# Optimization experiments

Measured on AMD Instinct MI355X. Metric: run time of the kernel, lower is better.

The kernel has to match this reference:

```python
import jax, jax.numpy as jnp
import numpy as np

N = 102400      # total agents across all groups
GROUP = 50      # agents per group
G = N // GROUP  # 2048 groups
E = 128         # embedding_dim
H = 512         # h_dim


def setup_inputs() -> dict:
    key = jax.random.key(0)
    k1, k2, k3, k4, k5, k6 = jax.random.split(key, 6)
    hist_enc = jax.random.normal(k1, (N, H), dtype=jnp.float32)
    hist_pos_batch = jax.random.normal(k2, (N, 2), dtype=jnp.float32)
    # group boundaries: 0, 50, 100, ..., N  (len = G+1)
    seq_start_end = (jnp.arange(G + 1, dtype=jnp.int32) * GROUP)
    # spatial_embedding: Linear(2, E)
    Ws = jax.random.normal(k3, (2, E), dtype=jnp.float32) * (1.0 / np.sqrt(2.0))
    bs = jax.random.normal(k4, (E,), dtype=jnp.float32) * 0.01
    # mlp_pre_pool: Linear(E + H, H)
    Wm = jax.random.normal(k5, (E + H, H), dtype=jnp.float32) * (1.0 / np.sqrt(E + H))
    bm = jax.random.normal(k6, (H,), dtype=jnp.float32) * 0.01
    return {
        "hist_enc": hist_enc,
        "hist_pos_batch": hist_pos_batch,
        "seq_start_end": seq_start_end,
        "Ws": Ws, "bs": bs, "Wm": Wm, "bm": bm,
    }


def reference(hist_enc, hist_pos_batch, seq_start_end, Ws, bs, Wm, bm):
    # The original torch loop builds all n^2 pairs per group but keeps only
    # curr_pool_h[0:1], i.e. row i=0 -> pooled vector for the group's FIRST agent.
    # rel[i=0, j] = pos[j] - pos[start]; hidden index is j; max over j.
    n = hist_enc.shape[0]
    num_groups = seq_start_end.shape[0] - 1
    # segment id of each agent: group g covers [sse[g], sse[g+1])
    seg_ids = jnp.searchsorted(seq_start_end, jnp.arange(n, dtype=seq_start_end.dtype), side="right") - 1
    starts = seq_start_end[:-1]                      # [G]
    anchor = hist_pos_batch[starts][seg_ids]         # [N,2] pos of group's first agent
    rel = hist_pos_batch - anchor                    # [N,2]
    emb = jax.nn.relu(rel @ Ws + bs)                 # [N,E]
    h_in = jnp.concatenate([hist_enc, emb], axis=1)  # [N,E+H]
    pooled = jax.nn.relu(h_in @ Wm + bm)             # [N,H]
    out = jax.ops.segment_max(pooled, seg_ids, num_segments=num_groups)  # [G,H]
    return out
```

## Files before the change

### kernel.cpp

```cpp
#include <hip/hip_runtime.h>


typedef __bf16 bf16x8 __attribute__((ext_vector_type(8)));
typedef float floatx4 __attribute__((ext_vector_type(4)));

constexpr int NR = 102400;
constexpr int NG = 2048;
constexpr int E  = 128;
constexpr int H  = 512;
constexpr int KD = 640;
constexpr int BM = 128, BN = 128, BK = 32;

__device__ inline unsigned short f2bf(float f) {
    unsigned u = __float_as_uint(f);
    u += 0x7FFF + ((u >> 16) & 1u);
    return (unsigned short)(u >> 16);
}

__device__ inline unsigned pk2(float lo, float hi) {
    return __builtin_amdgcn_perm(__float_as_uint(hi) + 0x8000u,
                                 __float_as_uint(lo) + 0x8000u, 0x07060302u);
}

__device__ inline void async16(const void* g, void* l) {
    __builtin_amdgcn_global_load_lds(
        (const __attribute__((address_space(1))) unsigned int*)g,
        (__attribute__((address_space(3))) unsigned int*)l, 16, 0, 0);
}

__global__ __launch_bounds__(256) void prep2(
    const float* __restrict__ hist_enc, const float* __restrict__ pos,
    const int* __restrict__ sse, const float* __restrict__ Ws,
    const float* __restrict__ bs, const float* __restrict__ Wm,
    unsigned short* __restrict__ WmT, unsigned short* __restrict__ Abf,
    int* __restrict__ segArr, int doAbf)
{
    const int b = blockIdx.x;
    const int t = threadIdx.x;
    if (doAbf && b < 3200) {
        __shared__ float relRow[32][2];
        const int rowBase = b * 32;
        if (t < 32) {
            const int i = rowBase + t;
            int l = 0, r = NG + 1;
            while (l < r) { int m = (l + r) >> 1; if (sse[m] <= i) l = m + 1; else r = m; }
            const int g = l - 1;
            if (segArr) segArr[i] = g;
            const int a = sse[g];
            relRow[t][0] = pos[2 * i + 0] - pos[2 * a + 0];
            relRow[t][1] = pos[2 * i + 1] - pos[2 * a + 1];
        }
        __syncthreads();
#pragma unroll
        for (int j = 0; j < 8; ++j) {
            const int c = j * 256 + t;
            const int row = c >> 6, col = (c & 63) * 8;
            const float4 f0 = *(const float4*)&hist_enc[(size_t)(rowBase + row) * H + col];
            const float4 f1 = *(const float4*)&hist_enc[(size_t)(rowBase + row) * H + col + 4];
            uint4 u;
            u.x = pk2(f0.x, f0.y); u.y = pk2(f0.z, f0.w);
            u.z = pk2(f1.x, f1.y); u.w = pk2(f1.z, f1.w);
            *(uint4*)&Abf[(size_t)(rowBase + row) * KD + col] = u;
        }
#pragma unroll
        for (int j = 0; j < 2; ++j) {
            const int c = j * 256 + t;
            const int row = c >> 4, e = (c & 15) * 8;
            const float r0 = relRow[row][0], r1 = relRow[row][1];
            const float4 w0a = *(const float4*)&Ws[e],     w0b = *(const float4*)&Ws[e + 4];
            const float4 w1a = *(const float4*)&Ws[E + e], w1b = *(const float4*)&Ws[E + e + 4];
            const float4 ba  = *(const float4*)&bs[e],     bb  = *(const float4*)&bs[e + 4];
            const float v0 = fmaxf(r0 * w0a.x + r1 * w1a.x + ba.x, 0.f);
            const float v1 = fmaxf(r0 * w0a.y + r1 * w1a.y + ba.y, 0.f);
            const float v2 = fmaxf(r0 * w0a.z + r1 * w1a.z + ba.z, 0.f);
            const float v3 = fmaxf(r0 * w0a.w + r1 * w1a.w + ba.w, 0.f);
            const float v4 = fmaxf(r0 * w0b.x + r1 * w1b.x + bb.x, 0.f);
            const float v5 = fmaxf(r0 * w0b.y + r1 * w1b.y + bb.y, 0.f);
            const float v6 = fmaxf(r0 * w0b.z + r1 * w1b.z + bb.z, 0.f);
            const float v7 = fmaxf(r0 * w0b.w + r1 * w1b.w + bb.w, 0.f);
            uint4 u;
            u.x = pk2(v0, v1); u.y = pk2(v2, v3);
            u.z = pk2(v4, v5); u.w = pk2(v6, v7);
            *(uint4*)&Abf[(size_t)(rowBase + row) * KD + H + e] = u;
        }
    } else {
        const int bb = doAbf ? (b - 3200) : b;
        if (bb < 0 || bb >= 80) return;
        __shared__ float tile[64][65];
        const int kb = (bb % 10) * 64, nb = (bb / 10) * 64;
        const int tx = t & 63, tq = t >> 6;
#pragma unroll
        for (int i = 0; i < 16; ++i) {
            const int k = tq * 16 + i;
            tile[k][tx] = Wm[(size_t)(kb + k) * H + nb + tx];
        }
        __syncthreads();
#pragma unroll
        for (int i = 0; i < 16; ++i) {
            const int n = tq * 16 + i;
            WmT[(size_t)(nb + n) * KD + kb + tx] = f2bf(tile[tx][n]);
        }
    }
}

__global__ __launch_bounds__(256) void pool_mfma6(
    const unsigned short* __restrict__ Abf,
    const int*   __restrict__ sse,
    const int*   __restrict__ segArr,
    const unsigned short* __restrict__ WmT,
    const float* __restrict__ bm,
    float*       __restrict__ out)
{
    __shared__ __attribute__((aligned(16))) unsigned short As2[2][BM * BK];
    __shared__ __attribute__((aligned(16))) unsigned short Bs2[2][BN * BK];
    __shared__ int segRow[BM];
    __shared__ int bnd[3];
    __shared__ int Pmax[4][BN + 4];

    const int t = threadIdx.x;
    const int bid     = blockIdx.x;
    const int rowTile = (bid >> 5) * 8 + (bid & 7);
    const int colTile = (bid >> 3) & 3;
    const int rowBase = rowTile * BM;
    const int cTile   = colTile * BN;

    const int lane  = t & 63;
    const int wv    = t >> 6;
    const int wr    = (wv >> 1) * 64;
    const int wc    = (wv & 1) * 64;
    const int lcol  = lane & 15;
    const int lquad = lane >> 4;

    const int sRow0 = wv * 32 + (lane >> 2);
    const int sRow1 = sRow0 + 16;
    const int phys  = lane & 3;
    const int cl0   = phys ^ ((sRow0 >> 1) & 3);
    const int cl1   = phys ^ ((sRow1 >> 1) & 3);
    const unsigned short* gA0 = Abf + (size_t)(rowBase + sRow0) * KD + cl0 * 8;
    const unsigned short* gA1 = Abf + (size_t)(rowBase + sRow1) * KD + cl1 * 8;
    const unsigned short* gB0 = WmT + (size_t)(cTile + sRow0) * KD + cl0 * 8;
    const unsigned short* gB1 = WmT + (size_t)(cTile + sRow1) * KD + cl1 * 8;

    auto issue = [&](int kt, int buf) {
        const int ko = kt * BK;
        async16(gA0 + ko, &As2[buf][wv * 1024]);
        async16(gA1 + ko, &As2[buf][wv * 1024 + 512]);
        async16(gB0 + ko, &Bs2[buf][wv * 1024]);
        async16(gB1 + ko, &Bs2[buf][wv * 1024 + 512]);
    };

    issue(0, 0);

    if (segArr) {
        if (t < BM) segRow[t] = segArr[rowBase + t];
    } else if (t < BM) {
        const int i = rowBase + t;
        int l = 0, r = NG + 1;
        while (l < r) { int m = (l + r) >> 1; if (sse[m] <= i) l = m + 1; else r = m; }
        segRow[t] = l - 1;
    }
    if (t >= BM && t < BM + 3) bnd[t - BM] = BM;
    for (int idx = t; idx < 4 * (BN + 4); idx += 256) ((int*)Pmax)[idx] = 0;
    __syncthreads();
    if (t < BM - 1) {
        const int s0 = segRow[t], s1 = segRow[t + 1];
        if (s1 != s0) bnd[s1 - segRow[0] - 1] = t + 1;
    }

    floatx4 acc[4][4];
#pragma unroll
    for (int m = 0; m < 4; ++m)
#pragma unroll
        for (int n = 0; n < 4; ++n) acc[m][n] = (floatx4){0.f, 0.f, 0.f, 0.f};

    for (int kt = 0; kt < KD / BK; ++kt) {
        __syncthreads();
        if (kt < KD / BK - 1) issue(kt + 1, (kt + 1) & 1);

        const unsigned short* A = As2[kt & 1];
        const unsigned short* B = Bs2[kt & 1];
        bf16x8 af[4], bfr[4];
#pragma unroll
        for (int mt = 0; mt < 4; ++mt) {
            const int R = wr + mt * 16 + lcol;
            const int pc = lquad ^ ((R >> 1) & 3);
            af[mt] = *(const bf16x8*)&A[R * 32 + pc * 8];
        }
#pragma unroll
        for (int nt = 0; nt < 4; ++nt) {
            const int R = wc + nt * 16 + lcol;
            const int pc = lquad ^ ((R >> 1) & 3);
            bfr[nt] = *(const bf16x8*)&B[R * 32 + pc * 8];
        }
#pragma unroll
        for (int mt = 0; mt < 4; ++mt)
#pragma unroll
            for (int nt = 0; nt < 4; ++nt)
                acc[mt][nt] = __builtin_amdgcn_mfma_f32_16x16x32_bf16(af[mt], bfr[nt], acc[mt][nt], 0, 0, 0);
    }

    const int b0 = bnd[0], b1 = bnd[1], b2 = bnd[2];
    const int segBase = segRow[0];

#pragma unroll
    for (int nt = 0; nt < 4; ++nt) {
        const int col  = wc + nt * 16 + lcol;
        const float bias = bm[cTile + col];
        float pm[4] = {0.f, 0.f, 0.f, 0.f};
#pragma unroll
        for (int mt = 0; mt < 4; ++mt) {
#pragma unroll
            for (int r = 0; r < 4; ++r) {
                const int lr = wr + mt * 16 + lquad * 4 + r;
                const int ls = (lr >= b0) + (lr >= b1) + (lr >= b2);
                const float v = fmaxf(acc[mt][nt][r] + bias, 0.f);
                pm[ls] = fmaxf(pm[ls], v);
            }
        }
#pragma unroll
        for (int ls = 0; ls < 4; ++ls)
            if (pm[ls] > 0.f)
                atomicMax(&Pmax[ls][col], __float_as_int(pm[ls]));
    }
    __syncthreads();

    for (int idx = t; idx < 4 * BN; idx += 256) {
        const int ls = idx >> 7, col = idx & 127;
        if (ls > 0 && bnd[ls - 1] >= BM) continue;
        const int seg = segBase + ls;
        const int v   = Pmax[ls][col];
        const int gs  = sse[seg], ge = sse[seg + 1];
        float* dst = &out[(size_t)seg * H + cTile + col];
        if (gs >= rowBase && ge <= rowBase + BM) {
            *dst = __int_as_float(v);
        } else {
            atomicMax((int*)dst, v);
        }
    }
}

constexpr int LDAF = 40;
__global__ __launch_bounds__(256) void pool_mfma_fb(
    const float* __restrict__ hist_enc, const float* __restrict__ pos,
    const int* __restrict__ sse, const float* __restrict__ Ws,
    const float* __restrict__ bs, const unsigned short* __restrict__ WmT,
    const float* __restrict__ bm, float* __restrict__ out)
{
    __shared__ __attribute__((aligned(16))) unsigned short As[BM][LDAF];
    __shared__ __attribute__((aligned(16))) unsigned short Bs[BN][LDAF];
    __shared__ float relRow[BM][2];
    __shared__ int   segRow[BM];
    __shared__ int   bnd[3];
    __shared__ int   Pmax[4][BN + 4];

    const int t = threadIdx.x;
    const int cTile = blockIdx.x * BN;
    const int rowBase = blockIdx.y * BM;

    if (t < BM) {
        const int i = rowBase + t;
        int l = 0, r = NG + 1;
        while (l < r) { int m = (l + r) >> 1; if (sse[m] <= i) l = m + 1; else r = m; }
        const int g = l - 1;
        segRow[t] = g;
        const int a = sse[g];
        relRow[t][0] = pos[2 * i + 0] - pos[2 * a + 0];
        relRow[t][1] = pos[2 * i + 1] - pos[2 * a + 1];
    }
    if (t >= BM && t < BM + 3) bnd[t - BM] = BM;
    for (int idx = t; idx < 4 * (BN + 4); idx += 256) ((int*)Pmax)[idx] = 0;
    __syncthreads();
    if (t < BM - 1) {
        const int s0 = segRow[t], s1 = segRow[t + 1];
        if (s1 != s0) bnd[s1 - segRow[0] - 1] = t + 1;
    }

    const int lane = t & 63, wv = t >> 6;
    const int wr = (wv >> 1) * 64, wc = (wv & 1) * 64;
    const int lcol = lane & 15, lquad = lane >> 4;

    floatx4 acc[4][4];
#pragma unroll
    for (int m = 0; m < 4; ++m)
#pragma unroll
        for (int n = 0; n < 4; ++n) acc[m][n] = (floatx4){0.f, 0.f, 0.f, 0.f};

    for (int kt = 0; kt < KD / BK; ++kt) {
        const int k0 = kt * BK;
        float4 av[4]; uint4 bv[2];
        if (k0 < H) {
#pragma unroll
            for (int i = 0; i < 4; ++i) {
                const int idx = i * 256 + t;
                const int row = idx >> 3, kq = (idx & 7) * 4;
                av[i] = *(const float4*)&hist_enc[(size_t)(rowBase + row) * H + k0 + kq];
            }
        } else {
#pragma unroll
            for (int i = 0; i < 4; ++i) {
                const int idx = i * 256 + t;
                const int row = idx >> 3, kq = (idx & 7) * 4;
                const int e = k0 - H + kq;
                const float4 w0 = *(const float4*)&Ws[e];
                const float4 w1 = *(const float4*)&Ws[E + e];
                const float4 b4 = *(const float4*)&bs[e];
                const float r0 = relRow[row][0], r1 = relRow[row][1];
                av[i].x = fmaxf(r0 * w0.x + r1 * w1.x + b4.x, 0.f);
                av[i].y = fmaxf(r0 * w0.y + r1 * w1.y + b4.y, 0.f);
                av[i].z = fmaxf(r0 * w0.z + r1 * w1.z + b4.z, 0.f);
                av[i].w = fmaxf(r0 * w0.w + r1 * w1.w + b4.w, 0.f);
            }
        }
#pragma unroll
        for (int i = 0; i < 2; ++i) {
            const int idx = i * 256 + t;
            const int n = idx >> 2, q = idx & 3;
            bv[i] = *(const uint4*)&WmT[(size_t)(cTile + n) * KD + k0 + q * 8];
        }
        __syncthreads();
#pragma unroll
        for (int i = 0; i < 4; ++i) {
            const int idx = i * 256 + t;
            const int row = idx >> 3, kq = (idx & 7) * 4;
            ushort4 p;
            p.x = f2bf(av[i].x); p.y = f2bf(av[i].y);
            p.z = f2bf(av[i].z); p.w = f2bf(av[i].w);
            *(ushort4*)&As[row][kq] = p;
        }
#pragma unroll
        for (int i = 0; i < 2; ++i) {
            const int idx = i * 256 + t;
            const int n = idx >> 2, q = idx & 3;
            *(uint4*)&Bs[n][q * 8] = bv[i];
        }
        __syncthreads();

        bf16x8 af[4], bfr[4];
#pragma unroll
        for (int mt = 0; mt < 4; ++mt)
            af[mt] = *(const bf16x8*)&As[wr + mt * 16 + lcol][lquad * 8];
#pragma unroll
        for (int nt = 0; nt < 4; ++nt)
            bfr[nt] = *(const bf16x8*)&Bs[wc + nt * 16 + lcol][lquad * 8];
#pragma unroll
        for (int mt = 0; mt < 4; ++mt)
#pragma unroll
            for (int nt = 0; nt < 4; ++nt)
                acc[mt][nt] = __builtin_amdgcn_mfma_f32_16x16x32_bf16(af[mt], bfr[nt], acc[mt][nt], 0, 0, 0);
    }

    const int b0 = bnd[0], b1 = bnd[1], b2 = bnd[2];
    const int segBase = segRow[0];
#pragma unroll
    for (int nt = 0; nt < 4; ++nt) {
        const int col = wc + nt * 16 + lcol;
        const float bias = bm[cTile + col];
        float pm[4] = {0.f, 0.f, 0.f, 0.f};
#pragma unroll
        for (int mt = 0; mt < 4; ++mt) {
#pragma unroll
            for (int r = 0; r < 4; ++r) {
                const int lr = wr + mt * 16 + lquad * 4 + r;
                const int ls = (lr >= b0) + (lr >= b1) + (lr >= b2);
                const float v = fmaxf(acc[mt][nt][r] + bias, 0.f);
                pm[ls] = fmaxf(pm[ls], v);
            }
        }
#pragma unroll
        for (int ls = 0; ls < 4; ++ls)
            if (pm[ls] > 0.f) atomicMax(&Pmax[ls][col], __float_as_int(pm[ls]));
    }
    __syncthreads();
    for (int idx = t; idx < 4 * BN; idx += 256) {
        const int ls = idx >> 7, col = idx & 127;
        if (ls > 0 && bnd[ls - 1] >= BM) continue;
        const int seg = segBase + ls;
        const int v = Pmax[ls][col];
        const int gs = sse[seg], ge = sse[seg + 1];
        float* dst = &out[(size_t)seg * H + cTile + col];
        if (gs >= rowBase && ge <= rowBase + BM) *dst = __int_as_float(v);
        else atomicMax((int*)dst, v);
    }
}

extern "C" void kernel_launch(void* const* d_in, const int* in_sizes, int n_in,
                              void* d_out, int out_size, void* d_ws, size_t ws_size,
                              hipStream_t stream) {
    const float* hist_enc = (const float*)d_in[0];
    const float* pos      = (const float*)d_in[1];
    const int*   sse      = (const int*)  d_in[2];
    const float* Ws       = (const float*)d_in[3];
    const float* bs       = (const float*)d_in[4];
    const float* Wm       = (const float*)d_in[5];
    const float* bm       = (const float*)d_in[6];
    float*       out      = (float*)d_out;

    const size_t needWmT = (size_t)H * KD * 2;
    const size_t needA   = (size_t)NR * KD * 2;
    const size_t needSeg = (size_t)NR * 4;
    unsigned short* WmT  = (unsigned short*)d_ws;
    unsigned short* Abf  = (unsigned short*)((char*)d_ws + needWmT);
    int*            segA = (int*)((char*)d_ws + needWmT + needA);

    hipMemsetAsync(out, 0, (size_t)out_size * sizeof(float), stream);

    if (ws_size >= needWmT + needA + needSeg) {
        prep2<<<3280, 256, 0, stream>>>(hist_enc, pos, sse, Ws, bs, Wm, WmT, Abf, segA, 1);
        pool_mfma6<<<3200, 256, 0, stream>>>(Abf, sse, segA, WmT, bm, out);
    } else if (ws_size >= needWmT + needA) {
        prep2<<<3280, 256, 0, stream>>>(hist_enc, pos, sse, Ws, bs, Wm, WmT, Abf, nullptr, 1);
        pool_mfma6<<<3200, 256, 0, stream>>>(Abf, sse, nullptr, WmT, bm, out);
    } else {
        prep2<<<80, 256, 0, stream>>>(hist_enc, pos, sse, Ws, bs, Wm, WmT, Abf, nullptr, 0);
        pool_mfma_fb<<<dim3(H / BN, NR / BM), 256, 0, stream>>>(hist_enc, pos, sse, Ws, bs, WmT, bm, out);
    }
}
```

Baseline: 432.7 us.

## Fuse bf16 conversion and spatial embedding into GEMM A-tile loading

Removes the intermediate bf16 A matrix (N x 640) that was written by a prep kernel and re-read by the GEMM. The GEMM now loads fp32 hist_enc directly, converts it to bf16 in registers and stores it into LDS. It computes the spatial-embedding columns on the fly from precomputed relative positions. Tiles change to 64x256 with all four waves sharing the A rows, and occupancy is hinted at 3 blocks. In exchange, each A tile is reread twice across the two column tiles in fp32 and conversion ALU work moves inside the main loop.

New measurement: 412.8 us. 1.05x faster.

```diff
diff --git a/kernel.cpp b/kernel.cpp
--- a/kernel.cpp
+++ b/kernel.cpp
@@ -10,6 +10,9 @@
 constexpr int H  = 512;
 constexpr int KD = 640;
 constexpr int BM = 128, BN = 128, BK = 32;
+constexpr int FM = 64, FN = 256;
+constexpr int NKT = KD / BK;
+constexpr int KH  = H / BK;
 
 __device__ inline unsigned short f2bf(float f) {
     unsigned u = __float_as_uint(f);
@@ -28,65 +31,26 @@
         (__attribute__((address_space(3))) unsigned int*)l, 16, 0, 0);
 }
 
-__global__ __launch_bounds__(256) void prep2(
-    const float* __restrict__ hist_enc, const float* __restrict__ pos,
-    const int* __restrict__ sse, const float* __restrict__ Ws,
-    const float* __restrict__ bs, const float* __restrict__ Wm,
-    unsigned short* __restrict__ WmT, unsigned short* __restrict__ Abf,
-    int* __restrict__ segArr, int doAbf)
+__global__ __launch_bounds__(256) void prep3(
+    const float* __restrict__ pos, const int* __restrict__ sse,
+    const float* __restrict__ Wm, unsigned short* __restrict__ WmT,
+    int* __restrict__ segArr, float* __restrict__ relA)
 {
     const int b = blockIdx.x;
     const int t = threadIdx.x;
-    if (doAbf && b < 3200) {
-        __shared__ float relRow[32][2];
-        const int rowBase = b * 32;
-        if (t < 32) {
-            const int i = rowBase + t;
-            int l = 0, r = NG + 1;
-            while (l < r) { int m = (l + r) >> 1; if (sse[m] <= i) l = m + 1; else r = m; }
-            const int g = l - 1;
-            if (segArr) segArr[i] = g;
-            const int a = sse[g];
-            relRow[t][0] = pos[2 * i + 0] - pos[2 * a + 0];
-            relRow[t][1] = pos[2 * i + 1] - pos[2 * a + 1];
-        }
-        __syncthreads();
-#pragma unroll
-        for (int j = 0; j < 8; ++j) {
-            const int c = j * 256 + t;
-            const int row = c >> 6, col = (c & 63) * 8;
-            const float4 f0 = *(const float4*)&hist_enc[(size_t)(rowBase + row) * H + col];
-            const float4 f1 = *(const float4*)&hist_enc[(size_t)(rowBase + row) * H + col + 4];
-            uint4 u;
-            u.x = pk2(f0.x, f0.y); u.y = pk2(f0.z, f0.w);
-            u.z = pk2(f1.x, f1.y); u.w = pk2(f1.z, f1.w);
-            *(uint4*)&Abf[(size_t)(rowBase + row) * KD + col] = u;
-        }
-#pragma unroll
-        for (int j = 0; j < 2; ++j) {
-            const int c = j * 256 + t;
-            const int row = c >> 4, e = (c & 15) * 8;
-            const float r0 = relRow[row][0], r1 = relRow[row][1];
-            const float4 w0a = *(const float4*)&Ws[e],     w0b = *(const float4*)&Ws[e + 4];
-            const float4 w1a = *(const float4*)&Ws[E + e], w1b = *(const float4*)&Ws[E + e + 4];
-            const float4 ba  = *(const float4*)&bs[e],     bb  = *(const float4*)&bs[e + 4];
-            const float v0 = fmaxf(r0 * w0a.x + r1 * w1a.x + ba.x, 0.f);
-            const float v1 = fmaxf(r0 * w0a.y + r1 * w1a.y + ba.y, 0.f);
-            const float v2 = fmaxf(r0 * w0a.z + r1 * w1a.z + ba.z, 0.f);
-            const float v3 = fmaxf(r0 * w0a.w + r1 * w1a.w + ba.w, 0.f);
-            const float v4 = fmaxf(r0 * w0b.x + r1 * w1b.x + bb.x, 0.f);
-            const float v5 = fmaxf(r0 * w0b.y + r1 * w1b.y + bb.y, 0.f);
-            const float v6 = fmaxf(r0 * w0b.z + r1 * w1b.z + bb.z, 0.f);
-            const float v7 = fmaxf(r0 * w0b.w + r1 * w1b.w + bb.w, 0.f);
-            uint4 u;
-            u.x = pk2(v0, v1); u.y = pk2(v2, v3);
-            u.z = pk2(v4, v5); u.w = pk2(v6, v7);
-            *(uint4*)&Abf[(size_t)(rowBase + row) * KD + H + e] = u;
-        }
+    __shared__ float tile[64][65];
+    if (b < 400) {
+        if (!segArr) return;
+        const int i = b * 256 + t;
+        int l = 0, r = NG + 1;
+        while (l < r) { int m = (l + r) >> 1; if (sse[m] <= i) l = m + 1; else r = m; }
+        const int g = l - 1;
+        segArr[i] = g;
+        const int a = sse[g];
+        relA[2 * i + 0] = pos[2 * i + 0] - pos[2 * a + 0];
+        relA[2 * i + 1] = pos[2 * i + 1] - pos[2 * a + 1];
     } else {
-        const int bb = doAbf ? (b - 3200) : b;
-        if (bb < 0 || bb >= 80) return;
-        __shared__ float tile[64][65];
+        const int bb = b - 400;
         const int kb = (bb % 10) * 64, nb = (bb / 10) * 64;
         const int tx = t & 63, tq = t >> 6;
 #pragma unroll
@@ -103,66 +67,76 @@
     }
 }
 
-__global__ __launch_bounds__(256) void pool_mfma6(
-    const unsigned short* __restrict__ Abf,
+__global__ __launch_bounds__(256, 3) void pool_fused(
+    const float* __restrict__ hist_enc,
     const int*   __restrict__ sse,
     const int*   __restrict__ segArr,
+    const float* __restrict__ relA,
+    const float* __restrict__ Ws,
+    const float* __restrict__ bs,
     const unsigned short* __restrict__ WmT,
     const float* __restrict__ bm,
     float*       __restrict__ out)
 {
-    __shared__ __attribute__((aligned(16))) unsigned short As2[2][BM * BK];
-    __shared__ __attribute__((aligned(16))) unsigned short Bs2[2][BN * BK];
-    __shared__ int segRow[BM];
+    __shared__ __attribute__((aligned(16))) unsigned short As2[2][FM * BK];
+    __shared__ __attribute__((aligned(16))) unsigned short Bs2[2][FN * BK];
+    __shared__ float2 relRow[FM];
+    __shared__ int segRow[FM];
     __shared__ int bnd[3];
-    __shared__ int Pmax[4][BN + 4];
-
-    const int t = threadIdx.x;
-    const int bid     = blockIdx.x;
-    const int rowTile = (bid >> 5) * 8 + (bid & 7);
-    const int colTile = (bid >> 3) & 3;
-    const int rowBase = rowTile * BM;
-    const int cTile   = colTile * BN;
+    __shared__ int Pmax[4][FN + 4];
+
+    const int t   = threadIdx.x;
+    const int bid = blockIdx.x;
+    const int rowTile = (bid >> 4) * 8 + (bid & 7);
+    const int colTile = (bid >> 3) & 1;
+    const int rowBase = rowTile * FM;
+    const int cTile   = colTile * FN;
 
     const int lane  = t & 63;
     const int wv    = t >> 6;
-    const int wr    = (wv >> 1) * 64;
-    const int wc    = (wv & 1) * 64;
+    const int wc    = wv * 64;
     const int lcol  = lane & 15;
     const int lquad = lane >> 4;
 
-    const int sRow0 = wv * 32 + (lane >> 2);
-    const int sRow1 = sRow0 + 16;
-    const int phys  = lane & 3;
-    const int cl0   = phys ^ ((sRow0 >> 1) & 3);
-    const int cl1   = phys ^ ((sRow1 >> 1) & 3);
-    const unsigned short* gA0 = Abf + (size_t)(rowBase + sRow0) * KD + cl0 * 8;
-    const unsigned short* gA1 = Abf + (size_t)(rowBase + sRow1) * KD + cl1 * 8;
-    const unsigned short* gB0 = WmT + (size_t)(cTile + sRow0) * KD + cl0 * 8;
-    const unsigned short* gB1 = WmT + (size_t)(cTile + sRow1) * KD + cl1 * 8;
-
-    auto issue = [&](int kt, int buf) {
+    const int sR   = lane >> 2;
+    const int phys = lane & 3;
+    const unsigned short* gB[4];
+#pragma unroll
+    for (int s = 0; s < 4; ++s) {
+        const int row = wv * 64 + s * 16 + sR;
+        const int cl  = phys ^ ((row >> 1) & 3);
+        gB[s] = WmT + (size_t)(cTile + row) * KD + cl * 8;
+    }
+    auto issueB = [&](int kt, int buf) {
         const int ko = kt * BK;
-        async16(gA0 + ko, &As2[buf][wv * 1024]);
-        async16(gA1 + ko, &As2[buf][wv * 1024 + 512]);
-        async16(gB0 + ko, &Bs2[buf][wv * 1024]);
-        async16(gB1 + ko, &Bs2[buf][wv * 1024 + 512]);
+#pragma unroll
+        for (int s = 0; s < 4; ++s)
+            async16(gB[s] + ko, &Bs2[buf][wv * 2048 + s * 512]);
     };
 
-    issue(0, 0);
-
-    if (segArr) {
-        if (t < BM) segRow[t] = segArr[rowBase + t];
-    } else if (t < BM) {
-        const int i = rowBase + t;
-        int l = 0, r = NG + 1;
-        while (l < r) { int m = (l + r) >> 1; if (sse[m] <= i) l = m + 1; else r = m; }
-        segRow[t] = l - 1;
-    }
-    if (t >= BM && t < BM + 3) bnd[t - BM] = BM;
-    for (int idx = t; idx < 4 * (BN + 4); idx += 256) ((int*)Pmax)[idx] = 0;
+    const int arow = t >> 2, ach = t & 3;
+    const int aoff = arow * BK + (ach ^ ((arow >> 1) & 3)) * 8;
+    const float* gA = hist_enc + (size_t)(rowBase + arow) * H + ach * 8;
+
+    issueB(0, 0);
+
+    if (t < FM) {
+        segRow[t] = segArr[rowBase + t];
+        relRow[t] = *(const float2*)&relA[2 * (rowBase + t)];
+    }
+    if (t >= FM && t < FM + 3) bnd[t - FM] = FM;
+    for (int idx = t; idx < 4 * (FN + 4); idx += 256) ((int*)Pmax)[idx] = 0;
+
+    {
+        const float4 h0 = *(const float4*)(gA);
+        const float4 h1 = *(const float4*)(gA + 4);
+        uint4 u;
+        u.x = pk2(h0.x, h0.y); u.y = pk2(h0.z, h0.w);
+        u.z = pk2(h1.x, h1.y); u.w = pk2(h1.z, h1.w);
+        *(uint4*)&As2[0][aoff] = u;
+    }
     __syncthreads();
-    if (t < BM - 1) {
+    if (t < FM - 1) {
         const int s0 = segRow[t], s1 = segRow[t + 1];
         if (s1 != s0) bnd[s1 - segRow[0] - 1] = t + 1;
     }
@@ -173,30 +147,68 @@
 #pragma unroll
         for (int n = 0; n < 4; ++n) acc[m][n] = (floatx4){0.f, 0.f, 0.f, 0.f};
 
-    for (int kt = 0; kt < KD / BK; ++kt) {
+    for (int kt = 0; kt < NKT; ++kt) {
         __syncthreads();
-        if (kt < KD / BK - 1) issue(kt + 1, (kt + 1) & 1);
+        const int nxt = kt + 1;
+        float4 w0a, w0b, w1a, w1b, ba, bb;
+        float r0 = 0.f, r1 = 0.f;
+        bool hist = true;
+        if (nxt < NKT) {
+            issueB(nxt, nxt & 1);
+            if (nxt < KH) {
+                w0a = *(const float4*)(gA + nxt * BK);
+                w0b = *(const float4*)(gA + nxt * BK + 4);
+            } else {
+                hist = false;
+                const int e0 = nxt * BK - H + ach * 8;
+                w0a = *(const float4*)&Ws[e0];     w0b = *(const float4*)&Ws[e0 + 4];
+                w1a = *(const float4*)&Ws[E + e0]; w1b = *(const float4*)&Ws[E + e0 + 4];
+                ba  = *(const float4*)&bs[e0];     bb  = *(const float4*)&bs[e0 + 4];
+                const float2 rr = relRow[arow];
+                r0 = rr.x; r1 = rr.y;
+            }
+        }
 
         const unsigned short* A = As2[kt & 1];
         const unsigned short* B = Bs2[kt & 1];
         bf16x8 af[4], bfr[4];
 #pragma unroll
         for (int mt = 0; mt < 4; ++mt) {
-            const int R = wr + mt * 16 + lcol;
+            const int R  = mt * 16 + lcol;
             const int pc = lquad ^ ((R >> 1) & 3);
-            af[mt] = *(const bf16x8*)&A[R * 32 + pc * 8];
+            af[mt] = *(const bf16x8*)&A[R * BK + pc * 8];
         }
 #pragma unroll
         for (int nt = 0; nt < 4; ++nt) {
-            const int R = wc + nt * 16 + lcol;
+            const int R  = wc + nt * 16 + lcol;
             const int pc = lquad ^ ((R >> 1) & 3);
-            bfr[nt] = *(const bf16x8*)&B[R * 32 + pc * 8];
+            bfr[nt] = *(const bf16x8*)&B[R * BK + pc * 8];
         }
 #pragma unroll
         for (int mt = 0; mt < 4; ++mt)
 #pragma unroll
             for (int nt = 0; nt < 4; ++nt)
                 acc[mt][nt] = __builtin_amdgcn_mfma_f32_16x16x32_bf16(af[mt], bfr[nt], acc[mt][nt], 0, 0, 0);
+
+        if (nxt < NKT) {
+            uint4 u;
+            if (hist) {
+                u.x = pk2(w0a.x, w0a.y); u.y = pk2(w0a.z, w0a.w);
+                u.z = pk2(w0b.x, w0b.y); u.w = pk2(w0b.z, w0b.w);
+            } else {
+                const float v0 = fmaxf(r0 * w0a.x + r1 * w1a.x + ba.x, 0.f);
+                const float v1 = fmaxf(r0 * w0a.y + r1 * w1a.y + ba.y, 0.f);
+                const float v2 = fmaxf(r0 * w0a.z + r1 * w1a.z + ba.z, 0.f);
+                const float v3 = fmaxf(r0 * w0a.w + r1 * w1a.w + ba.w, 0.f);
+                const float v4 = fmaxf(r0 * w0b.x + r1 * w1b.x + bb.x, 0.f);
+                const float v5 = fmaxf(r0 * w0b.y + r1 * w1b.y + bb.y, 0.f);
+                const float v6 = fmaxf(r0 * w0b.z + r1 * w1b.z + bb.z, 0.f);
+                const float v7 = fmaxf(r0 * w0b.w + r1 * w1b.w + bb.w, 0.f);
+                u.x = pk2(v0, v1); u.y = pk2(v2, v3);
+                u.z = pk2(v4, v5); u.w = pk2(v6, v7);
+            }
+            *(uint4*)&As2[nxt & 1][aoff] = u;
+        }
     }
 
     const int b0 = bnd[0], b1 = bnd[1], b2 = bnd[2];
@@ -211,7 +223,7 @@
         for (int mt = 0; mt < 4; ++mt) {
 #pragma unroll
             for (int r = 0; r < 4; ++r) {
-                const int lr = wr + mt * 16 + lquad * 4 + r;
+                const int lr = mt * 16 + lquad * 4 + r;
                 const int ls = (lr >= b0) + (lr >= b1) + (lr >= b2);
                 const float v = fmaxf(acc[mt][nt][r] + bias, 0.f);
                 pm[ls] = fmaxf(pm[ls], v);
@@ -224,14 +236,14 @@
     }
     __syncthreads();
 
-    for (int idx = t; idx < 4 * BN; idx += 256) {
-        const int ls = idx >> 7, col = idx & 127;
-        if (ls > 0 && bnd[ls - 1] >= BM) continue;
+    for (int idx = t; idx < 4 * FN; idx += 256) {
+        const int ls = idx >> 8, col = idx & (FN - 1);
+        if (ls > 0 && bnd[ls - 1] >= FM) continue;
         const int seg = segBase + ls;
         const int v   = Pmax[ls][col];
         const int gs  = sse[seg], ge = sse[seg + 1];
         float* dst = &out[(size_t)seg * H + cTile + col];
-        if (gs >= rowBase && ge <= rowBase + BM) {
+        if (gs >= rowBase && ge <= rowBase + FM) {
             *dst = __int_as_float(v);
         } else {
             atomicMax((int*)dst, v);
@@ -396,22 +408,19 @@
     float*       out      = (float*)d_out;
 
     const size_t needWmT = (size_t)H * KD * 2;
-    const size_t needA   = (size_t)NR * KD * 2;
     const size_t needSeg = (size_t)NR * 4;
+    const size_t needRel = (size_t)NR * 2 * 4;
     unsigned short* WmT  = (unsigned short*)d_ws;
-    unsigned short* Abf  = (unsigned short*)((char*)d_ws + needWmT);
-    int*            segA = (int*)((char*)d_ws + needWmT + needA);
+    int*            segA = (int*)  ((char*)d_ws + needWmT);
+    float*          relA = (float*)((char*)d_ws + needWmT + needSeg);
 
     hipMemsetAsync(out, 0, (size_t)out_size * sizeof(float), stream);
 
-    if (ws_size >= needWmT + needA + needSeg) {
-        prep2<<<3280, 256, 0, stream>>>(hist_enc, pos, sse, Ws, bs, Wm, WmT, Abf, segA, 1);
-        pool_mfma6<<<3200, 256, 0, stream>>>(Abf, sse, segA, WmT, bm, out);
-    } else if (ws_size >= needWmT + needA) {
-        prep2<<<3280, 256, 0, stream>>>(hist_enc, pos, sse, Ws, bs, Wm, WmT, Abf, nullptr, 1);
-        pool_mfma6<<<3200, 256, 0, stream>>>(Abf, sse, nullptr, WmT, bm, out);
+    if (ws_size >= needWmT + needSeg + needRel) {
+        prep3<<<480, 256, 0, stream>>>(pos, sse, Wm, WmT, segA, relA);
+        pool_fused<<<3200, 256, 0, stream>>>(hist_enc, sse, segA, relA, Ws, bs, WmT, bm, out);
     } else {
-        prep2<<<80, 256, 0, stream>>>(hist_enc, pos, sse, Ws, bs, Wm, WmT, Abf, nullptr, 0);
+        prep3<<<480, 256, 0, stream>>>(pos, sse, Wm, WmT, nullptr, nullptr);
         pool_mfma_fb<<<dim3(H / BN, NR / BM), 256, 0, stream>>>(hist_enc, pos, sse, Ws, bs, WmT, bm, out);
     }
 }
```
